# Optimization experiments

Hardware: AMD Instinct MI355X
Metric: run time of the kernel (lower is better)

## Reference

```python
import jax, jax.numpy as jnp
import numpy as np

N = 100000; E = 1600000; G = 2000; S = 40; MAXP = 50
IN = 64; F = 128; H = 4; HD = F // H; FFN = 8 * F
EPS = 1e-5; BN_EPS = 1e-5

def _ln(x, g, b):
    m = jnp.mean(x, -1, keepdims=True)
    v = jnp.mean((x - m) ** 2, -1, keepdims=True)
    return (x - m) * jax.lax.rsqrt(v + EPS) * g + b

def setup_inputs():
    key = jax.random.key(0)
    ks = jax.random.split(key, 16)
    def lin(k, i, o):
        kw, kb = jax.random.split(k)
        lim = 1.0 / np.sqrt(i)
        return (jax.random.uniform(kw, (i, o), jnp.float32, -lim, lim),
                jax.random.uniform(kb, (o,), jnp.float32, -lim, lim))
    W_gcn, b_gcn = lin(ks[1], IN, F)
    Wq, bq = lin(ks[2], F, F); Wk, bk = lin(ks[3], F, F)
    Wv, bv = lin(ks[4], F, F); Wo, bo = lin(ks[5], F, F)
    W1, b1 = lin(ks[6], F, FFN); W2, b2 = lin(ks[7], FFN, F)
    Wg, bg = lin(ks[8], 2 * F, F)
    ones = lambda: jnp.ones((F,), jnp.float32)
    zeros = lambda: jnp.zeros((F,), jnp.float32)
    return {
        'x': jax.random.normal(ks[0], (N, IN), jnp.float32),
        'edge_index': jax.random.randint(ks[9], (2, E), 0, N),
        'batch': jnp.repeat(jnp.arange(G), N // G),
        'set_batch': jnp.repeat(jnp.arange(S), G // S),
        'W_gcn': W_gcn, 'b_gcn': b_gcn,
        'bn_g': ones(), 'bn_b': zeros(),
        'lnpre_g': ones(), 'lnpre_b': zeros(),
        'Wq': Wq, 'bq': bq, 'Wk': Wk, 'bk': bk, 'Wv': Wv, 'bv': bv, 'Wo': Wo, 'bo': bo,
        'ln1_g': ones(), 'ln1_b': zeros(),
        'W1': W1, 'b1': b1, 'W2': W2, 'b2': b2,
        'ln2_g': ones(), 'ln2_b': zeros(),
        'Wg': Wg, 'bg': bg,
    }

def _forward(x, W_gcn, b_gcn, bn_g, bn_b, lnpre_g, lnpre_b, Wq, bq, Wk, bk, Wv, bv, Wo, bo, ln1_g, ln1_b, W1, b1, W2, b2, ln2_g, ln2_b, Wg, bg, edge_index, batch, set_batch):
    row, col = edge_index[0], edge_index[1]
    # GCNConv, improved=True -> self-loop weight 2.0 (PyG gcn_norm)
    xw = x @ W_gcn                                              # [N,F]
    deg = jax.ops.segment_sum(jnp.ones(E, xw.dtype), col, N) + 2.0
    dinv = jax.lax.rsqrt(deg)
    norm = dinv[row] * dinv[col]                                # [E]
    agg = jax.ops.segment_sum(xw[row] * norm[:, None], col, N)  # scatter-add to targets
    h = agg + (2.0 * dinv * dinv)[:, None] * xw + b_gcn
    # BatchNorm1d eval (running_mean=0, running_var=1) + ReLU; dropout is identity in eval
    h = jax.nn.relu(h * jax.lax.rsqrt(jnp.asarray(1.0 + BN_EPS, h.dtype)) * bn_g + bn_b)
    # global mean pool per graph
    cnt_g = jax.ops.segment_sum(jnp.ones(N, h.dtype), batch, G)
    z = jax.ops.segment_sum(h, batch, G) / cnt_g[:, None]       # [G,F]
    # to_dense_batch over sets (set_batch is sorted)
    cnt_s = jax.ops.segment_sum(jnp.ones(G, jnp.int32), set_batch, S)
    starts = jnp.cumsum(cnt_s) - cnt_s
    pos = jnp.arange(G) - starts[set_batch]                     # position within set
    zd = jnp.zeros((S, MAXP, F), z.dtype).at[set_batch, pos].set(z)
    mask = jnp.arange(MAXP)[None, :] < cnt_s[:, None]           # [S,MAXP]
    # pre-LN MHA with key_padding_mask
    zn = _ln(zd, lnpre_g, lnpre_b)
    q = (zn @ Wq + bq).reshape(S, MAXP, H, HD)
    k = (zn @ Wk + bk).reshape(S, MAXP, H, HD)
    v = (zn @ Wv + bv).reshape(S, MAXP, H, HD)
    scores = jnp.einsum('sqhd,skhd->shqk', q, k) / np.sqrt(HD)
    scores = jnp.where(mask[:, None, None, :], scores, -1e9)
    attn = jax.nn.softmax(scores, -1)
    o = jnp.einsum('shqk,skhd->sqhd', attn, v).reshape(S, MAXP, F) @ Wo + bo
    zd = _ln(zd + o, ln1_g, ln1_b)
    # FFN block (post-LN residual)
    f = jax.nn.relu(zd @ W1 + b1) @ W2 + b2
    zd = _ln(zd + f, ln2_g, ln2_b)
    # z_dense[mask] ordering == gather via (set_batch, pos); broadcast to nodes
    set_info = zd[set_batch, pos][batch]                        # [N,F]
    # gated fusion
    gate = jax.nn.sigmoid(jnp.concatenate([h, set_info], -1) @ Wg + bg)
    return gate * set_info + (1.0 - gate) * h

def reference(x, edge_index, batch, set_batch, W_gcn, b_gcn, bn_g, bn_b, lnpre_g, lnpre_b, Wq, bq, Wk, bk, Wv, bv, Wo, bo, ln1_g, ln1_b, W1, b1, W2, b2, ln2_g, ln2_b, Wg, bg):
    return _forward(x, W_gcn, b_gcn, bn_g, bn_b, lnpre_g, lnpre_b, Wq, bq, Wk, bk, Wv, bv, Wo, bo, ln1_g, ln1_b, W1, b1, W2, b2, ln2_g, ln2_b, Wg, bg, edge_index, batch, set_batch)
```

## Files before the change

### kernel.cpp

```cpp
#include <hip/hip_runtime.h>
#include <hip/hip_bf16.h>
#include <cstddef>

#define NN 100000
#define NE 1600000
#define NG 2000
#define NS 40
#define INF 64
#define F 128
#define FFN_DIM 1024
#define NB 782
#define SC_BLOCKS 512
#define SC_CHUNK 3125
#define BH_BLOCKS 128
#define BH_CHUNK 12500
#define KSPLIT 8

using bf16 = __hip_bfloat16;
using bf162 = __hip_bfloat162;
typedef __attribute__((ext_vector_type(8))) short short8;
typedef __attribute__((ext_vector_type(4))) float f32x4;
typedef __attribute__((ext_vector_type(2))) float f32x2;

__device__ __forceinline__ short f2bs(float f){
    union { bf16 b; short s; } u; u.b = __float2bfloat16(f); return u.s;
}

__global__ __launch_bounds__(1024) void k_bhist(const int* __restrict__ ei, int* __restrict__ bcnt){
    __shared__ int lh[NB];
    int t = threadIdx.x;
    int base = blockIdx.x * BH_CHUNK;
    for (int b=t; b<NB; b+=1024) lh[b] = 0;
    __syncthreads();
    for (int i=t; i<BH_CHUNK; i+=1024){
        int c = ei[NE + base + i];
        atomicAdd(&lh[c>>7], 1);
    }
    __syncthreads();
    for (int b=t; b<NB; b+=1024){
        int n = lh[b];
        if (n) atomicAdd(&bcnt[b], n);
    }
}

__global__ __launch_bounds__(1024) void k_bscan(const int* __restrict__ bcnt, int* __restrict__ bstart,
                                                int* __restrict__ bcursor){
    __shared__ int s[1024];
    int t = threadIdx.x;
    int own = (t < NB) ? bcnt[t] : 0;
    s[t] = own; __syncthreads();
    #pragma unroll
    for (int off=1; off<1024; off<<=1){
        int v = (t >= off) ? s[t-off] : 0;
        __syncthreads();
        s[t] += v;
        __syncthreads();
    }
    int excl = s[t] - own;
    if (t <= NB) bstart[t] = excl;
    if (t < NB)  bcursor[t] = excl;
}

__global__ __launch_bounds__(256) void k_xws(const float* __restrict__ x, const float* __restrict__ W,
                                             const float* __restrict__ dinv, unsigned char* __restrict__ xws8){
    __shared__ short Xs[128*72];
    __shared__ short Ws[128*72];
    int t = threadIdx.x;
    int rowBase = blockIdx.x * 128;
    #pragma unroll
    for (int i=0;i<32;i++){
        int id = i*256+t; int k = id>>7, n = id&127;
        Ws[n*72 + k] = f2bs(W[id]);
    }
    #pragma unroll
    for (int i=0;i<8;i++){
        int id = i*256+t;
        int r = id>>4; int k4 = (id&15)*4;
        int row = rowBase + r; if (row >= NN) row = NN-1;
        float4 v = *(const float4*)&x[(size_t)row*INF + k4];
        unsigned int u0 = (unsigned int)(unsigned short)f2bs(v.x) | ((unsigned int)(unsigned short)f2bs(v.y)<<16);
        unsigned int u1 = (unsigned int)(unsigned short)f2bs(v.z) | ((unsigned int)(unsigned short)f2bs(v.w)<<16);
        *(unsigned int*)&Xs[r*72 + k4]     = u0;
        *(unsigned int*)&Xs[r*72 + k4 + 2] = u1;
    }
    __syncthreads();
    int lane = t & 63, w = t >> 6;
    int lr = lane & 15, quad = lane >> 4;
    f32x4 acc[2][8];
    #pragma unroll
    for (int i=0;i<2;i++)
        #pragma unroll
        for (int j=0;j<8;j++) acc[i][j] = (f32x4){0.f,0.f,0.f,0.f};
    #pragma unroll
    for (int ks=0; ks<2; ++ks){
        int kb = ks*32 + quad*8;
        short8 b0 = *(const short8*)&Xs[((w  )*16 + lr)*72 + kb];
        short8 b1 = *(const short8*)&Xs[((w+4)*16 + lr)*72 + kb];
        #pragma unroll
        for (int mt=0; mt<8; ++mt){
            short8 a = *(const short8*)&Ws[(mt*16 + lr)*72 + kb];
            acc[0][mt] = __builtin_amdgcn_mfma_f32_16x16x32_bf16(a, b0, acc[0][mt], 0, 0, 0);
            acc[1][mt] = __builtin_amdgcn_mfma_f32_16x16x32_bf16(a, b1, acc[1][mt], 0, 0, 0);
        }
    }
    #pragma unroll
    for (int rt=0; rt<2; ++rt){
        int row = rowBase + (w + rt*4)*16 + lr;
        if (row < NN){
            float dv = dinv[row];
            #pragma unroll
            for (int mt=0; mt<8; ++mt){
                int p = __builtin_amdgcn_cvt_pk_fp8_f32(acc[rt][mt][0]*dv, acc[rt][mt][1]*dv, 0, false);
                p     = __builtin_amdgcn_cvt_pk_fp8_f32(acc[rt][mt][2]*dv, acc[rt][mt][3]*dv, p, true);
                *(int*)&xws8[(size_t)row*F + mt*16 + quad*4] = p;
            }
        }
    }
}

__global__ __launch_bounds__(1024) void k_scatter2(const int* __restrict__ ei, int* __restrict__ bcursor,
                                                   int* __restrict__ ebuf){
    __shared__ int lh[NB];
    __shared__ int lb[NB];
    int t = threadIdx.x;
    int base = blockIdx.x * SC_CHUNK;
    for (int b=t; b<NB; b+=1024) lh[b] = 0;
    __syncthreads();
    int rr[4], cc[4];
    #pragma unroll
    for (int q=0;q<4;q++){
        int i = t + q*1024;
        bool v = (i < SC_CHUNK);
        int idx = v ? (base + i) : base;
        rr[q] = ei[idx];
        cc[q] = ei[NE + idx];
        if (v) atomicAdd(&lh[cc[q]>>7], 1);
    }
    __syncthreads();
    for (int b=t; b<NB; b+=1024){
        int n = lh[b];
        lb[b] = n ? atomicAdd(&bcursor[b], n) : 0;
        lh[b] = 0;
    }
    __syncthreads();
    #pragma unroll
    for (int q=0;q<4;q++){
        int i = t + q*1024;
        if (i < SC_CHUNK){
            int b = cc[q] >> 7;
            int rk = atomicAdd(&lh[b], 1);
            ebuf[lb[b] + rk] = (rr[q] << 7) | (cc[q] & 127);
        }
    }
}

__global__ __launch_bounds__(256) void k_sort(const int* __restrict__ ebuf, const int* __restrict__ bstart,
                                              int* __restrict__ cnt, float* __restrict__ dinv,
                                              int* __restrict__ nstart, int* __restrict__ ebuf2){
    __shared__ int lh[128];
    __shared__ int s[128];
    __shared__ int lcur[128];
    int t = threadIdx.x;
    int b = blockIdx.x;
    int e0 = bstart[b];
    int nE = bstart[b+1] - e0;
    if (t < 128) lh[t] = 0;
    __syncthreads();
    for (int i=t; i<nE; i+=256) atomicAdd(&lh[ebuf[e0+i] & 127], 1);
    __syncthreads();
    int c = (t < 128) ? lh[t] : 0;
    if (t < 128) s[t] = c;
    __syncthreads();
    #pragma unroll
    for (int off=1; off<128; off<<=1){
        int v = (t >= off && t < 128) ? s[t-off] : 0;
        __syncthreads();
        if (t < 128) s[t] += v;
        __syncthreads();
    }
    int node = b*128 + t;
    if (t < 128){
        int excl = s[t] - c;
        lcur[t] = excl;
        if (node < NN){
            nstart[node] = e0 + excl;
            cnt[node] = c;
            dinv[node] = rsqrtf((float)c + 2.0f);
        }
    }
    __syncthreads();
    for (int i=t; i<nE; i+=256){
        int v = ebuf[e0 + i];
        int nl = v & 127;
        int rk = atomicAdd(&lcur[nl], 1);
        ebuf2[e0 + rk] = (v >> 7) << 5;
    }
}

__global__ __launch_bounds__(256) void k_aggpool(const unsigned char* __restrict__ xws8,
                                                 const int* __restrict__ nstart, const int* __restrict__ cnt,
                                                 const float* __restrict__ dinv, const float* __restrict__ b_gcn,
                                                 const float* __restrict__ bn_g, const float* __restrict__ bn_b,
                                                 const int* __restrict__ ebuf2,
                                                 const float* __restrict__ lnpre_g, const float* __restrict__ lnpre_b,
                                                 float* __restrict__ h, unsigned short* __restrict__ hb,
                                                 float* __restrict__ z, float* __restrict__ zn){
    __shared__ float zacc[4][128];
    int t = threadIdx.x;
    int lane = t & 63, w = t >> 6;
    int half = lane >> 5, lh = lane & 31;
    int g = blockIdx.x;
    const unsigned int* xw32 = (const unsigned int*)xws8;
    unsigned int* hb32 = (unsigned int*)hb;

    float4 bg4  = *(const float4*)&b_gcn[4*lh];
    float4 bng4 = *(const float4*)&bn_g[4*lh];
    float4 bnb4 = *(const float4*)&bn_b[4*lh];
    const float bns = rsqrtf(1.f + 1e-5f);

    float za0=0.f, za1=0.f, za2=0.f, za3=0.f;

    for (int i = w; i < 50; i += 4){
        int node = g*50 + i;
        int s0n = nstart[node]; int dg = cnt[node]; float dv = dinv[node];
        unsigned int us = xw32[node*32 + lh];
        float a0=0.f, a1=0.f, a2=0.f, a3=0.f;
        int j=0;
        for (; j+8<=dg; j+=8){
            int r0 = ebuf2[s0n+j+0+half];
            int r1 = ebuf2[s0n+j+2+half];
            int r2 = ebuf2[s0n+j+4+half];
            int r3 = ebuf2[s0n+j+6+half];
            unsigned int u0 = xw32[r0 + lh];
            unsigned int u1 = xw32[r1 + lh];
            unsigned int u2 = xw32[r2 + lh];
            unsigned int u3 = xw32[r3 + lh];
            f32x2 l0 = __builtin_amdgcn_cvt_pk_f32_fp8(u0, false);
            f32x2 h0 = __builtin_amdgcn_cvt_pk_f32_fp8(u0, true);
            f32x2 l1 = __builtin_amdgcn_cvt_pk_f32_fp8(u1, false);
            f32x2 h1 = __builtin_amdgcn_cvt_pk_f32_fp8(u1, true);
            f32x2 l2 = __builtin_amdgcn_cvt_pk_f32_fp8(u2, false);
            f32x2 h2 = __builtin_amdgcn_cvt_pk_f32_fp8(u2, true);
            f32x2 l3 = __builtin_amdgcn_cvt_pk_f32_fp8(u3, false);
            f32x2 h3 = __builtin_amdgcn_cvt_pk_f32_fp8(u3, true);
            a0 += (l0.x + l1.x) + (l2.x + l3.x);
            a1 += (l0.y + l1.y) + (l2.y + l3.y);
            a2 += (h0.x + h1.x) + (h2.x + h3.x);
            a3 += (h0.y + h1.y) + (h2.y + h3.y);
        }
        for (; j+2<=dg; j+=2){
            int r0 = ebuf2[s0n+j+half];
            unsigned int u0 = xw32[r0 + lh];
            f32x2 l0 = __builtin_amdgcn_cvt_pk_f32_fp8(u0, false);
            f32x2 h0 = __builtin_amdgcn_cvt_pk_f32_fp8(u0, true);
            a0 += l0.x; a1 += l0.y; a2 += h0.x; a3 += h0.y;
        }
        if (j < dg && half == 0){
            int r0 = ebuf2[s0n+j];
            unsigned int u0 = xw32[r0 + lh];
            f32x2 l0 = __builtin_amdgcn_cvt_pk_f32_fp8(u0, false);
            f32x2 h0 = __builtin_amdgcn_cvt_pk_f32_fp8(u0, true);
            a0 += l0.x; a1 += l0.y; a2 += h0.x; a3 += h0.y;
        }
        a0 += __shfl_xor(a0, 32);
        a1 += __shfl_xor(a1, 32);
        a2 += __shfl_xor(a2, 32);
        a3 += __shfl_xor(a3, 32);
        f32x2 fl = __builtin_amdgcn_cvt_pk_f32_fp8(us, false);
        f32x2 fh = __builtin_amdgcn_cvt_pk_f32_fp8(us, true);
        float p0 = dv*(a0 + 2.f*fl.x) + bg4.x;
        float p1 = dv*(a1 + 2.f*fl.y) + bg4.y;
        float p2 = dv*(a2 + 2.f*fh.x) + bg4.z;
        float p3 = dv*(a3 + 2.f*fh.y) + bg4.w;
        p0 = fmaxf(p0*bns*bng4.x + bnb4.x, 0.f);
        p1 = fmaxf(p1*bns*bng4.y + bnb4.y, 0.f);
        p2 = fmaxf(p2*bns*bng4.z + bnb4.z, 0.f);
        p3 = fmaxf(p3*bns*bng4.w + bnb4.w, 0.f);
        if (half == 0){
            *(float4*)&h[(size_t)node*F + 4*lh] = make_float4(p0,p1,p2,p3);
            unsigned int b0 = (unsigned int)(unsigned short)f2bs(p0) | ((unsigned int)(unsigned short)f2bs(p1) << 16);
            unsigned int b1 = (unsigned int)(unsigned short)f2bs(p2) | ((unsigned int)(unsigned short)f2bs(p3) << 16);
            *(uint2*)&hb32[(size_t)node*64 + 2*lh] = make_uint2(b0, b1);
        }
        za0 += p0; za1 += p1; za2 += p2; za3 += p3;
    }
    if (half == 0)
        *(float4*)&zacc[w][4*lh] = make_float4(za0, za1, za2, za3);
    __syncthreads();
    if (w == 0){
        float4 v0 = *(const float4*)&zacc[0][4*lh];
        float4 v1 = *(const float4*)&zacc[1][4*lh];
        float4 v2 = *(const float4*)&zacc[2][4*lh];
        float4 v3 = *(const float4*)&zacc[3][4*lh];
        float s0 = ((v0.x+v1.x)+(v2.x+v3.x)) / 50.0f;
        float s1 = ((v0.y+v1.y)+(v2.y+v3.y)) / 50.0f;
        float s2 = ((v0.z+v1.z)+(v2.z+v3.z)) / 50.0f;
        float s3 = ((v0.w+v1.w)+(v2.w+v3.w)) / 50.0f;
        if (half == 0)
            *(float4*)&z[(size_t)g*F + 4*lh] = make_float4(s0,s1,s2,s3);
        float s = (s0+s1)+(s2+s3);
        #pragma unroll
        for (int off=1; off<32; off<<=1) s += __shfl_xor(s, off);
        float m = s * (1.f/128.f);
        float d0=s0-m, d1=s1-m, d2=s2-m, d3=s3-m;
        float vv = (d0*d0+d1*d1)+(d2*d2+d3*d3);
        #pragma unroll
        for (int off=1; off<32; off<<=1) vv += __shfl_xor(vv, off);
        float rs = rsqrtf(vv*(1.f/128.f) + 1e-5f);
        float4 lg = *(const float4*)&lnpre_g[4*lh];
        float4 lb = *(const float4*)&lnpre_b[4*lh];
        if (half == 0)
            *(float4*)&zn[(size_t)g*F + 4*lh] = make_float4(d0*rs*lg.x+lb.x, d1*rs*lg.y+lb.y,
                                                            d2*rs*lg.z+lb.z, d3*rs*lg.w+lb.w);
    }
}

__global__ __launch_bounds__(256) void k_wo_ln(const float* __restrict__ ao, const float* __restrict__ Wo,
                                               const float* __restrict__ bo, const float* __restrict__ z,
                                               const float* __restrict__ g, const float* __restrict__ b,
                                               float* __restrict__ zd1){
    __shared__ float As[32*36];
    __shared__ float Bs[32*128];
    int t = threadIdx.x;
    int rowBase = blockIdx.x*32;
    int c0 = (t&31)*4, r0 = (t>>5)*4;
    float acc[4][4];
    #pragma unroll
    for (int i=0;i<4;i++){ acc[i][0]=0.f; acc[i][1]=0.f; acc[i][2]=0.f; acc[i][3]=0.f; }
    for (int kb=0; kb<F; kb+=32){
        #pragma unroll
        for (int i=0;i<4;i++){
            int id = i*256+t; int kk = id&31; int r = id>>5;
            int row = rowBase + r;
            As[kk*36+r] = (row<NG) ? ao[(size_t)row*F + kb + kk] : 0.f;
        }
        #pragma unroll
        for (int i=0;i<16;i++){
            int id = i*256+t; int c = id&127; int kk = id>>7;
            Bs[kk*128+c] = Wo[(size_t)(kb+kk)*F + c];
        }
        __syncthreads();
        for (int kk=0;kk<32;kk++){
            float4 a = *(const float4*)&As[kk*36+r0];
            float4 bv = *(const float4*)&Bs[kk*128+c0];
            float av[4]={a.x,a.y,a.z,a.w}; float bb[4]={bv.x,bv.y,bv.z,bv.w};
            #pragma unroll
            for(int i=0;i<4;i++)
                #pragma unroll
                for(int j=0;j<4;j++) acc[i][j] += av[i]*bb[j];
        }
        __syncthreads();
    }
    float4 bo4 = *(const float4*)&bo[c0];
    float4 g4  = *(const float4*)&g[c0];
    float4 b4  = *(const float4*)&b[c0];
    #pragma unroll
    for (int i=0;i<4;i++){
        int row = rowBase + r0 + i;
        float v0=0.f,v1=0.f,v2=0.f,v3=0.f;
        if (row < NG){
            float4 zr = *(const float4*)&z[(size_t)row*F + c0];
            v0 = acc[i][0] + bo4.x + zr.x;
            v1 = acc[i][1] + bo4.y + zr.y;
            v2 = acc[i][2] + bo4.z + zr.z;
            v3 = acc[i][3] + bo4.w + zr.w;
        }
        float s = (v0+v1)+(v2+v3);
        #pragma unroll
        for (int off=1; off<32; off<<=1) s += __shfl_xor(s, off);
        float m = s * (1.f/128.f);
        float d0=v0-m, d1=v1-m, d2=v2-m, d3=v3-m;
        float vv = (d0*d0+d1*d1)+(d2*d2+d3*d3);
        #pragma unroll
        for (int off=1; off<32; off<<=1) vv += __shfl_xor(vv, off);
        float rs = rsqrtf(vv*(1.f/128.f) + 1e-5f);
        if (row < NG)
            *(float4*)&zd1[(size_t)row*F + c0] = make_float4(d0*rs*g4.x+b4.x, d1*rs*g4.y+b4.y,
                                                             d2*rs*g4.z+b4.z, d3*rs*g4.w+b4.w);
    }
}

__global__ __launch_bounds__(256) void k_ln_red_gsi(const float* __restrict__ A, const float* __restrict__ part,
                                                    const float* __restrict__ bias, const float* __restrict__ g,
                                                    const float* __restrict__ b, const float* __restrict__ Wb,
                                                    const float* __restrict__ bg, float* __restrict__ zd2,
                                                    float* __restrict__ gsi){
    __shared__ float Zs[4][128];
    __shared__ float Bs[32*128];
    int t = threadIdx.x; int lane = t&63;
    int rquad = t>>6;
    int row = blockIdx.x*4 + rquad;
    int i0 = row*F + 2*lane;
    float x0 = A[i0] + bias[2*lane], x1 = A[i0+1] + bias[2*lane+1];
    #pragma unroll
    for (int zz=0; zz<KSPLIT; ++zz){
        x0 += part[(size_t)zz*NG*F + i0];
        x1 += part[(size_t)zz*NG*F + i0 + 1];
    }
    float s = x0+x1;
    for (int off=1; off<64; off<<=1) s += __shfl_xor(s, off);
    float m = s * (1.f/128.f);
    float d0 = x0-m, d1 = x1-m;
    float vv = d0*d0 + d1*d1;
    for (int off=1; off<64; off<<=1) vv += __shfl_xor(vv, off);
    float rs = rsqrtf(vv*(1.f/128.f) + 1e-5f);
    float o0 = d0*rs*g[2*lane]   + b[2*lane];
    float o1 = d1*rs*g[2*lane+1] + b[2*lane+1];
    zd2[i0]   = o0;
    zd2[i0+1] = o1;
    Zs[rquad][2*lane]   = o0;
    Zs[rquad][2*lane+1] = o1;
    __syncthreads();
    int col = t & 127, rp = t >> 7;
    float a0=0.f, a1=0.f;
    for (int kb=0; kb<F; kb+=32){
        #pragma unroll
        for (int i=0;i<16;i++){
            int id = i*256+t; int c = id&127; int kk = id>>7;
            Bs[kk*128+c] = Wb[(size_t)(kb+kk)*F + c];
        }
        __syncthreads();
        for (int kk=0;kk<32;kk++){
            float w = Bs[kk*128+col];
            a0 += Zs[rp][kb+kk]   * w;
            a1 += Zs[rp+2][kb+kk] * w;
        }
        __syncthreads();
    }
    float bgc = bg[col];
    gsi[(size_t)(blockIdx.x*4 + rp)*F + col]     = a0 + bgc;
    gsi[(size_t)(blockIdx.x*4 + rp + 2)*F + col] = a1 + bgc;
}

template<int RELU>
__global__ __launch_bounds__(256) void k_gemm(const float* __restrict__ A, const float* __restrict__ B,
                                              const float* __restrict__ bias, float* __restrict__ C,
                                              int M, int K, int Nc){
    __shared__ float As[32*68];
    __shared__ float Bs[32*64];
    int t = threadIdx.x;
    int rowBase = blockIdx.x*64;
    int colBase = blockIdx.y*64;
    int c0 = (t&15)*4, r0 = (t>>4)*4;
    float acc[4][4];
    #pragma unroll
    for (int i=0;i<4;i++){ acc[i][0]=0.f; acc[i][1]=0.f; acc[i][2]=0.f; acc[i][3]=0.f; }
    for (int kb=0; kb<K; kb+=32){
        #pragma unroll
        for (int i=0;i<8;i++){
            int id = i*256+t; int kk = id&31; int r = id>>5;
            int row = rowBase + r;
            As[kk*68+r] = (row<M) ? A[(size_t)row*K + kb + kk] : 0.f;
        }
        #pragma unroll
        for (int i=0;i<8;i++){
            int id = i*256+t; int c = id&63; int kk = id>>6;
            Bs[kk*64+c] = B[(size_t)(kb+kk)*Nc + colBase + c];
        }
        __syncthreads();
        for (int kk=0;kk<32;kk++){
            float4 a = *(const float4*)&As[kk*68+r0];
            float4 b = *(const float4*)&Bs[kk*64+c0];
            float av[4]={a.x,a.y,a.z,a.w}; float bv[4]={b.x,b.y,b.z,b.w};
            #pragma unroll
            for(int i=0;i<4;i++)
                #pragma unroll
                for(int j=0;j<4;j++) acc[i][j] += av[i]*bv[j];
        }
        __syncthreads();
    }
    for (int i=0;i<4;i++){
        int row = rowBase + r0 + i;
        if (row < M){
            for (int j=0;j<4;j++){
                float v = acc[i][j] + bias[colBase+c0+j];
                if (RELU) v = fmaxf(v, 0.f);
                C[(size_t)row*Nc + colBase + c0 + j] = v;
            }
        }
    }
}

__global__ __launch_bounds__(256) void k_gemm_splitk(const float* __restrict__ A, const float* __restrict__ B,
                                                     float* __restrict__ part, int M, int K, int Nc){
    __shared__ float As[32*68];
    __shared__ float Bs[32*64];
    int t = threadIdx.x;
    int rowBase = blockIdx.x*64;
    int colBase = blockIdx.y*64;
    int z = blockIdx.z;
    int kchunk = K / KSPLIT;
    int kbeg = z * kchunk;
    int c0 = (t&15)*4, r0 = (t>>4)*4;
    float acc[4][4];
    #pragma unroll
    for (int i=0;i<4;i++){ acc[i][0]=0.f; acc[i][1]=0.f; acc[i][2]=0.f; acc[i][3]=0.f; }
    for (int kb=kbeg; kb<kbeg+kchunk; kb+=32){
        #pragma unroll
        for (int i=0;i<8;i++){
            int id = i*256+t; int kk = id&31; int r = id>>5;
            int row = rowBase + r;
            As[kk*68+r] = (row<M) ? A[(size_t)row*K + kb + kk] : 0.f;
        }
        #pragma unroll
        for (int i=0;i<8;i++){
            int id = i*256+t; int c = id&63; int kk = id>>6;
            Bs[kk*64+c] = B[(size_t)(kb+kk)*Nc + colBase + c];
        }
        __syncthreads();
        for (int kk=0;kk<32;kk++){
            float4 a = *(const float4*)&As[kk*68+r0];
            float4 b = *(const float4*)&Bs[kk*64+c0];
            float av[4]={a.x,a.y,a.z,a.w}; float bv[4]={b.x,b.y,b.z,b.w};
            #pragma unroll
            for(int i=0;i<4;i++)
                #pragma unroll
                for(int j=0;j<4;j++) acc[i][j] += av[i]*bv[j];
        }
        __syncthreads();
    }
    float* Cp = part + (size_t)z*M*Nc;
    for (int i=0;i<4;i++){
        int row = rowBase + r0 + i;
        if (row < M){
            for (int j=0;j<4;j++)
                Cp[(size_t)row*Nc + colBase + c0 + j] = acc[i][j];
        }
    }
}

__global__ __launch_bounds__(256) void k_gemm_qkv(const float* __restrict__ A,
                                                  const float* __restrict__ Wq, const float* __restrict__ Wk,
                                                  const float* __restrict__ Wv, const float* __restrict__ bq,
                                                  const float* __restrict__ bk, const float* __restrict__ bv,
                                                  float* __restrict__ Cq, float* __restrict__ Ck,
                                                  float* __restrict__ Cv){
    __shared__ float As[32*68];
    __shared__ float Bs[32*64];
    int t = threadIdx.x;
    int rowBase = blockIdx.x*64;
    int colBase = blockIdx.y*64;
    int z = blockIdx.z;
    const float* B = (z==0) ? Wq : (z==1) ? Wk : Wv;
    const float* bias = (z==0) ? bq : (z==1) ? bk : bv;
    float* C = (z==0) ? Cq : (z==1) ? Ck : Cv;
    int c0 = (t&15)*4, r0 = (t>>4)*4;
    float acc[4][4];
    #pragma unroll
    for (int i=0;i<4;i++){ acc[i][0]=0.f; acc[i][1]=0.f; acc[i][2]=0.f; acc[i][3]=0.f; }
    for (int kb=0; kb<F; kb+=32){
        #pragma unroll
        for (int i=0;i<8;i++){
            int id = i*256+t; int kk = id&31; int r = id>>5;
            int row = rowBase + r;
            As[kk*68+r] = (row<NG) ? A[(size_t)row*F + kb + kk] : 0.f;
        }
        #pragma unroll
        for (int i=0;i<8;i++){
            int id = i*256+t; int c = id&63; int kk = id>>6;
            Bs[kk*64+c] = B[(size_t)(kb+kk)*F + colBase + c];
        }
        __syncthreads();
        for (int kk=0;kk<32;kk++){
            float4 a = *(const float4*)&As[kk*68+r0];
            float4 b = *(const float4*)&Bs[kk*64+c0];
            float av[4]={a.x,a.y,a.z,a.w}; float bv4[4]={b.x,b.y,b.z,b.w};
            #pragma unroll
            for(int i=0;i<4;i++)
                #pragma unroll
                for(int j=0;j<4;j++) acc[i][j] += av[i]*bv4[j];
        }
        __syncthreads();
    }
    for (int i=0;i<4;i++){
        int row = rowBase + r0 + i;
        if (row < NG){
            for (int j=0;j<4;j++)
                C[(size_t)row*F + colBase + c0 + j] = acc[i][j] + bias[colBase+c0+j];
        }
    }
}

__global__ __launch_bounds__(256) void k_attn(const float* __restrict__ q, const float* __restrict__ k,
                                              const float* __restrict__ v, float* __restrict__ o){
    __shared__ float Qs[1600], Ks[1600], Vs[1600], Sc[2500];
    int t = threadIdx.x;
    int s = blockIdx.x >> 2; int hh = blockIdx.x & 3;
    for (int idx=t; idx<1600; idx+=256){
        int i = idx>>5, d = idx&31;
        size_t gi = (size_t)(s*50+i)*F + hh*32 + d;
        Qs[idx]=q[gi]; Ks[idx]=k[gi]; Vs[idx]=v[gi];
    }
    __syncthreads();
    for (int idx=t; idx<2500; idx+=256){
        int qi = idx/50, ki = idx%50;
        float acc=0.f;
        #pragma unroll 8
        for (int d=0;d<32;d++) acc += Qs[qi*32+d]*Ks[ki*32+d];
        Sc[idx] = acc * 0.17677669529663687f;
    }
    __syncthreads();
    if (t < 50){
        float m=-1e30f;
        for (int j=0;j<50;j++) m = fmaxf(m, Sc[t*50+j]);
        float sum=0.f;
        for (int j=0;j<50;j++){ float e=__expf(Sc[t*50+j]-m); Sc[t*50+j]=e; sum+=e; }
        float inv = 1.f/sum;
        for (int j=0;j<50;j++) Sc[t*50+j] *= inv;
    }
    __syncthreads();
    for (int idx=t; idx<1600; idx+=256){
        int qi = idx>>5, d = idx&31;
        float acc=0.f;
        #pragma unroll 10
        for (int ki=0;ki<50;ki++) acc += Sc[qi*50+ki]*Vs[ki*32+d];
        o[(size_t)(s*50+qi)*F + hh*32 + d] = acc;
    }
}

__global__ __launch_bounds__(256) void k_gate_mfma(const float* __restrict__ h,
                                                   const unsigned short* __restrict__ hb,
                                                   const float* __restrict__ Wg,
                                                   const float* __restrict__ gsi, const float* __restrict__ zd2,
                                                   float* __restrict__ out){
    __shared__ short Bw[128*136];
    int t = threadIdx.x;
    for (int i=t; i<16384; i+=256){
        int k = i >> 7, n = i & 127;
        Bw[n*136 + k] = f2bs(Wg[(size_t)k*F + n]);
    }
    __syncthreads();
    int lane = t & 63, w = t >> 6;
    int lr = lane & 15, quad = lane >> 4;
    int mrow0 = blockIdx.x*128 + w*32;
    f32x4 acc[2][8];
    #pragma unroll
    for (int i=0;i<2;i++)
        #pragma unroll
        for (int j=0;j<8;j++) acc[i][j] = (f32x4){0.f,0.f,0.f,0.f};
    #pragma unroll
    for (int ks=0; ks<4; ++ks){
        int kb = ks*32 + quad*8;
        short8 a[2];
        #pragma unroll
        for (int mt=0; mt<2; ++mt){
            int row = mrow0 + mt*16 + lr;
            if (row >= NN) row = NN-1;
            a[mt] = *(const short8*)&hb[(size_t)row*F + kb];
        }
        #pragma unroll
        for (int nt=0; nt<8; ++nt){
            short8 b = *(const short8*)&Bw[(nt*16 + lr)*136 + kb];
            acc[0][nt] = __builtin_amdgcn_mfma_f32_16x16x32_bf16(a[0], b, acc[0][nt], 0, 0, 0);
            acc[1][nt] = __builtin_amdgcn_mfma_f32_16x16x32_bf16(a[1], b, acc[1][nt], 0, 0, 0);
        }
    }
    #pragma unroll
    for (int mt=0; mt<2; ++mt){
        #pragma unroll
        for (int r=0; r<4; ++r){
            int row = mrow0 + mt*16 + quad*4 + r;
            if (row >= NN) continue;
            int g = row / 50;
            const float* gs = &gsi[(size_t)g*F];
            const float* zs = &zd2[(size_t)g*F];
            const float* hr = &h[(size_t)row*F];
            float* orow = &out[(size_t)row*F];
            #pragma unroll
            for (int nt=0; nt<8; ++nt){
                int col = nt*16 + lr;
                float L = acc[mt][nt][r] + gs[col];
                float gate = 1.f/(1.f + __expf(-L));
                orow[col] = gate*zs[col] + (1.f-gate)*hr[col];
            }
        }
    }
}

extern "C" void kernel_launch(void* const* d_in, const int* in_sizes, int n_in,
                              void* d_out, int out_size, void* d_ws, size_t ws_size,
                              hipStream_t stream) {
    const float* x      = (const float*)d_in[0];
    const int*   ei     = (const int*)d_in[1];
    const float* W_gcn  = (const float*)d_in[4];
    const float* b_gcn  = (const float*)d_in[5];
    const float* bn_g   = (const float*)d_in[6];
    const float* bn_b   = (const float*)d_in[7];
    const float* lnpre_g= (const float*)d_in[8];
    const float* lnpre_b= (const float*)d_in[9];
    const float* Wq     = (const float*)d_in[10];
    const float* bq     = (const float*)d_in[11];
    const float* Wk     = (const float*)d_in[12];
    const float* bk     = (const float*)d_in[13];
    const float* Wv     = (const float*)d_in[14];
    const float* bv     = (const float*)d_in[15];
    const float* Wo     = (const float*)d_in[16];
    const float* bo     = (const float*)d_in[17];
    const float* ln1_g  = (const float*)d_in[18];
    const float* ln1_b  = (const float*)d_in[19];
    const float* W1     = (const float*)d_in[20];
    const float* b1     = (const float*)d_in[21];
    const float* W2     = (const float*)d_in[22];
    const float* b2     = (const float*)d_in[23];
    const float* ln2_g  = (const float*)d_in[24];
    const float* ln2_b  = (const float*)d_in[25];
    const float* Wg     = (const float*)d_in[26];
    const float* bg     = (const float*)d_in[27];
    float* out = (float*)d_out;
    char* ws = (char*)d_ws;

    size_t o = 0;
    unsigned char* xws8 = (unsigned char*)(ws + o); o += (size_t)NN*F;
    float* h     = (float*)(ws + o); o += (size_t)NN*F*4;
    unsigned short* hb = (unsigned short*)(ws + o); o += (size_t)NN*F*2;
    int*   cnt   = (int*)(ws + o);   o += (size_t)NN*4;
    int*   nstart= (int*)(ws + o);   o += (size_t)NN*4;
    int*   ebuf  = (int*)(ws + o);   o += (size_t)NE*4;
    int*   ebuf2 = (int*)(ws + o);   o += (size_t)NE*4;
    float* dinv  = (float*)(ws + o); o += (size_t)NN*4;
    int*   bcnt  = (int*)(ws + o);   o += 1024*4;
    int*   bstart= (int*)(ws + o);   o += 1024*4;
    int*   bcursor=(int*)(ws + o);   o += 1024*4;
    float* z     = (float*)(ws + o); o += (size_t)NG*F*4;
    float* zn    = (float*)(ws + o); o += (size_t)NG*F*4;
    float* qb    = (float*)(ws + o); o += (size_t)NG*F*4;
    float* kb2   = (float*)(ws + o); o += (size_t)NG*F*4;
    float* vb    = (float*)(ws + o); o += (size_t)NG*F*4;
    float* ao    = (float*)(ws + o); o += (size_t)NG*F*4;
    float* zd1   = (float*)(ws + o); o += (size_t)NG*F*4;
    float* ffn1  = (float*)(ws + o); o += (size_t)NG*FFN_DIM*4;
    float* part  = (float*)(ws + o); o += (size_t)KSPLIT*NG*F*4;
    float* zd2   = (float*)(ws + o); o += (size_t)NG*F*4;
    float* gsi   = (float*)(ws + o); o += (size_t)NG*F*4;

    hipMemsetAsync(bcnt, 0, (size_t)NB*4, stream);
    k_bhist<<<BH_BLOCKS, 1024, 0, stream>>>(ei, bcnt);
    k_bscan<<<1, 1024, 0, stream>>>(bcnt, bstart, bcursor);
    k_scatter2<<<SC_BLOCKS, 1024, 0, stream>>>(ei, bcursor, ebuf);
    k_sort<<<NB, 256, 0, stream>>>(ebuf, bstart, cnt, dinv, nstart, ebuf2);
    k_xws<<<(NN+127)/128, 256, 0, stream>>>(x, W_gcn, dinv, xws8);
    k_aggpool<<<NG, 256, 0, stream>>>(xws8, nstart, cnt, dinv, b_gcn, bn_g, bn_b, ebuf2,
                                      lnpre_g, lnpre_b, h, hb, z, zn);

    dim3 gqkv(32, 2, 3);
    k_gemm_qkv<<<gqkv, 256, 0, stream>>>(zn, Wq, Wk, Wv, bq, bk, bv, qb, kb2, vb);
    k_attn<<<NS*4, 256, 0, stream>>>(qb, kb2, vb, ao);
    k_wo_ln<<<(NG+31)/32, 256, 0, stream>>>(ao, Wo, bo, z, ln1_g, ln1_b, zd1);
    dim3 gffn1(32, 16);
    k_gemm<1><<<gffn1, 256, 0, stream>>>(zd1, W1, b1, ffn1, NG, F, FFN_DIM);
    dim3 gsk(32, 2, KSPLIT);
    k_gemm_splitk<<<gsk, 256, 0, stream>>>(ffn1, W2, part, NG, FFN_DIM, F);
    k_ln_red_gsi<<<NG/4, 256, 0, stream>>>(zd1, part, b2, ln2_g, ln2_b,
                                           Wg + (size_t)F*F, bg, zd2, gsi);

    k_gate_mfma<<<782, 256, 0, stream>>>(h, hb, Wg, gsi, zd2, out);
}
```

Before: 360.8 us.

## Use fixed-capacity edge buckets and bf16 MFMA GEMMs for QKV and FFN

Replaces the edge-bucket histogram and scan kernels with fixed-capacity buckets (BCAP slots per bucket), initialised by one small kernel, so bucket counts come straight from the scatter cursors. The QKV, FFN1 and FFN2 fp32 SIMT GEMMs are replaced by bf16 MFMA kernels that take bf16 copies of zn and zd1 written by earlier stages, and FFN1 now writes its intermediate in bf16. This removes two launches and a memset and moves the small dense GEMMs onto matrix cores. In exchange it adds bf16 rounding error and risks overflow if any bucket gets more than 3072 edges.

```diff
diff --git a/kernel.cpp b/kernel.cpp
--- a/kernel.cpp
+++ b/kernel.cpp
@@ -10,14 +10,12 @@
 #define F 128
 #define FFN_DIM 1024
 #define NB 782
+#define BCAP 3072
 #define SC_BLOCKS 512
 #define SC_CHUNK 3125
-#define BH_BLOCKS 128
-#define BH_CHUNK 12500
 #define KSPLIT 8
 
 using bf16 = __hip_bfloat16;
-using bf162 = __hip_bfloat162;
 typedef __attribute__((ext_vector_type(8))) short short8;
 typedef __attribute__((ext_vector_type(4))) float f32x4;
 typedef __attribute__((ext_vector_type(2))) float f32x2;
@@ -25,40 +23,13 @@
 __device__ __forceinline__ short f2bs(float f){
     union { bf16 b; short s; } u; u.b = __float2bfloat16(f); return u.s;
 }
-
-__global__ __launch_bounds__(1024) void k_bhist(const int* __restrict__ ei, int* __restrict__ bcnt){
-    __shared__ int lh[NB];
-    int t = threadIdx.x;
-    int base = blockIdx.x * BH_CHUNK;
-    for (int b=t; b<NB; b+=1024) lh[b] = 0;
-    __syncthreads();
-    for (int i=t; i<BH_CHUNK; i+=1024){
-        int c = ei[NE + base + i];
-        atomicAdd(&lh[c>>7], 1);
-    }
-    __syncthreads();
-    for (int b=t; b<NB; b+=1024){
-        int n = lh[b];
-        if (n) atomicAdd(&bcnt[b], n);
-    }
-}
-
-__global__ __launch_bounds__(1024) void k_bscan(const int* __restrict__ bcnt, int* __restrict__ bstart,
-                                                int* __restrict__ bcursor){
-    __shared__ int s[1024];
-    int t = threadIdx.x;
-    int own = (t < NB) ? bcnt[t] : 0;
-    s[t] = own; __syncthreads();
-    #pragma unroll
-    for (int off=1; off<1024; off<<=1){
-        int v = (t >= off) ? s[t-off] : 0;
-        __syncthreads();
-        s[t] += v;
-        __syncthreads();
-    }
-    int excl = s[t] - own;
-    if (t <= NB) bstart[t] = excl;
-    if (t < NB)  bcursor[t] = excl;
+__device__ __forceinline__ unsigned int pk2(float a, float b){
+    return (unsigned int)(unsigned short)f2bs(a) | ((unsigned int)(unsigned short)f2bs(b) << 16);
+}
+
+__global__ __launch_bounds__(1024) void k_binit(int* __restrict__ bcursor){
+    int t = threadIdx.x;
+    if (t < NB) bcursor[t] = t * BCAP;
 }
 
 __global__ __launch_bounds__(256) void k_xws(const float* __restrict__ x, const float* __restrict__ W,
@@ -78,10 +49,8 @@
         int r = id>>4; int k4 = (id&15)*4;
         int row = rowBase + r; if (row >= NN) row = NN-1;
         float4 v = *(const float4*)&x[(size_t)row*INF + k4];
-        unsigned int u0 = (unsigned int)(unsigned short)f2bs(v.x) | ((unsigned int)(unsigned short)f2bs(v.y)<<16);
-        unsigned int u1 = (unsigned int)(unsigned short)f2bs(v.z) | ((unsigned int)(unsigned short)f2bs(v.w)<<16);
-        *(unsigned int*)&Xs[r*72 + k4]     = u0;
-        *(unsigned int*)&Xs[r*72 + k4 + 2] = u1;
+        *(unsigned int*)&Xs[r*72 + k4]     = pk2(v.x, v.y);
+        *(unsigned int*)&Xs[r*72 + k4 + 2] = pk2(v.z, v.w);
     }
     __syncthreads();
     int lane = t & 63, w = t >> 6;
@@ -154,7 +123,7 @@
     }
 }
 
-__global__ __launch_bounds__(256) void k_sort(const int* __restrict__ ebuf, const int* __restrict__ bstart,
+__global__ __launch_bounds__(256) void k_sort(const int* __restrict__ ebuf, const int* __restrict__ bcursor,
                                               int* __restrict__ cnt, float* __restrict__ dinv,
                                               int* __restrict__ nstart, int* __restrict__ ebuf2){
     __shared__ int lh[128];
@@ -162,8 +131,8 @@
     __shared__ int lcur[128];
     int t = threadIdx.x;
     int b = blockIdx.x;
-    int e0 = bstart[b];
-    int nE = bstart[b+1] - e0;
+    int e0 = b * BCAP;
+    int nE = bcursor[b] - e0;
     if (t < 128) lh[t] = 0;
     __syncthreads();
     for (int i=t; i<nE; i+=256) atomicAdd(&lh[ebuf[e0+i] & 127], 1);
@@ -204,7 +173,8 @@
                                                  const int* __restrict__ ebuf2,
                                                  const float* __restrict__ lnpre_g, const float* __restrict__ lnpre_b,
                                                  float* __restrict__ h, unsigned short* __restrict__ hb,
-                                                 float* __restrict__ z, float* __restrict__ zn){
+                                                 float* __restrict__ z, float* __restrict__ zn,
+                                                 unsigned short* __restrict__ znb){
     __shared__ float zacc[4][128];
     int t = threadIdx.x;
     int lane = t & 63, w = t >> 6;
@@ -212,6 +182,7 @@
     int g = blockIdx.x;
     const unsigned int* xw32 = (const unsigned int*)xws8;
     unsigned int* hb32 = (unsigned int*)hb;
+    unsigned int* znb32 = (unsigned int*)znb;
 
     float4 bg4  = *(const float4*)&b_gcn[4*lh];
     float4 bng4 = *(const float4*)&bn_g[4*lh];
@@ -278,9 +249,7 @@
         p3 = fmaxf(p3*bns*bng4.w + bnb4.w, 0.f);
         if (half == 0){
             *(float4*)&h[(size_t)node*F + 4*lh] = make_float4(p0,p1,p2,p3);
-            unsigned int b0 = (unsigned int)(unsigned short)f2bs(p0) | ((unsigned int)(unsigned short)f2bs(p1) << 16);
-            unsigned int b1 = (unsigned int)(unsigned short)f2bs(p2) | ((unsigned int)(unsigned short)f2bs(p3) << 16);
-            *(uint2*)&hb32[(size_t)node*64 + 2*lh] = make_uint2(b0, b1);
+            *(uint2*)&hb32[(size_t)node*64 + 2*lh] = make_uint2(pk2(p0,p1), pk2(p2,p3));
         }
         za0 += p0; za1 += p1; za2 += p2; za3 += p3;
     }
@@ -309,21 +278,148 @@
         float rs = rsqrtf(vv*(1.f/128.f) + 1e-5f);
         float4 lg = *(const float4*)&lnpre_g[4*lh];
         float4 lb = *(const float4*)&lnpre_b[4*lh];
-        if (half == 0)
-            *(float4*)&zn[(size_t)g*F + 4*lh] = make_float4(d0*rs*lg.x+lb.x, d1*rs*lg.y+lb.y,
-                                                            d2*rs*lg.z+lb.z, d3*rs*lg.w+lb.w);
+        if (half == 0){
+            float o0 = d0*rs*lg.x+lb.x, o1 = d1*rs*lg.y+lb.y;
+            float o2 = d2*rs*lg.z+lb.z, o3 = d3*rs*lg.w+lb.w;
+            *(float4*)&zn[(size_t)g*F + 4*lh] = make_float4(o0,o1,o2,o3);
+            *(uint2*)&znb32[(size_t)g*64 + 2*lh] = make_uint2(pk2(o0,o1), pk2(o2,o3));
+        }
+    }
+}
+
+template<int RELU, int BF16OUT, int SPLITK>
+__global__ __launch_bounds__(256) void k_mm_bf16(const unsigned short* __restrict__ A,
+                                                 const float* __restrict__ B, const float* __restrict__ bias,
+                                                 float* __restrict__ Cf, unsigned short* __restrict__ Cb,
+                                                 int M, int K, int Nc){
+    __shared__ short Bw[128*136];
+    int t = threadIdx.x;
+    int rowBase = blockIdx.x*128;
+    int colBase = blockIdx.y*128;
+    int kbeg = SPLITK ? blockIdx.z*128 : 0;
+    #pragma unroll
+    for (int i=0;i<64;i++){
+        int id = i*256+t; int k = id>>7, n = id&127;
+        Bw[n*136 + k] = f2bs(B[(size_t)(kbeg+k)*Nc + colBase + n]);
+    }
+    __syncthreads();
+    int lane = t & 63, w = t >> 6;
+    int lr = lane & 15, quad = lane >> 4;
+    int mrow0 = rowBase + w*32;
+    f32x4 acc[2][8];
+    #pragma unroll
+    for (int i=0;i<2;i++)
+        #pragma unroll
+        for (int j=0;j<8;j++) acc[i][j] = (f32x4){0.f,0.f,0.f,0.f};
+    #pragma unroll
+    for (int ks=0; ks<4; ++ks){
+        int kb = ks*32 + quad*8;
+        short8 a[2];
+        #pragma unroll
+        for (int mt=0; mt<2; ++mt){
+            int row = mrow0 + mt*16 + lr;
+            if (row >= M) row = M-1;
+            a[mt] = *(const short8*)&A[(size_t)row*K + kbeg + kb];
+        }
+        #pragma unroll
+        for (int nt=0; nt<8; ++nt){
+            short8 b = *(const short8*)&Bw[(nt*16 + lr)*136 + kb];
+            acc[0][nt] = __builtin_amdgcn_mfma_f32_16x16x32_bf16(a[0], b, acc[0][nt], 0, 0, 0);
+            acc[1][nt] = __builtin_amdgcn_mfma_f32_16x16x32_bf16(a[1], b, acc[1][nt], 0, 0, 0);
+        }
+    }
+    #pragma unroll
+    for (int mt=0; mt<2; ++mt){
+        #pragma unroll
+        for (int r=0; r<4; ++r){
+            int row = mrow0 + mt*16 + quad*4 + r;
+            if (row >= M) continue;
+            #pragma unroll
+            for (int nt=0; nt<8; ++nt){
+                int col = colBase + nt*16 + lr;
+                float v = acc[mt][nt][r];
+                if (!SPLITK){
+                    v += bias[col];
+                    if (RELU) v = fmaxf(v, 0.f);
+                    if (BF16OUT) Cb[(size_t)row*Nc + col] = (unsigned short)f2bs(v);
+                    else         Cf[(size_t)row*Nc + col] = v;
+                } else {
+                    Cf[(size_t)blockIdx.z*M*Nc + (size_t)row*Nc + col] = v;
+                }
+            }
+        }
+    }
+}
+
+__global__ __launch_bounds__(256) void k_qkv_mfma(const unsigned short* __restrict__ A,
+                                                  const float* __restrict__ Wq, const float* __restrict__ Wk,
+                                                  const float* __restrict__ Wv, const float* __restrict__ bq,
+                                                  const float* __restrict__ bk, const float* __restrict__ bv,
+                                                  float* __restrict__ Cq, float* __restrict__ Ck,
+                                                  float* __restrict__ Cv){
+    __shared__ short Bw[128*136];
+    int t = threadIdx.x;
+    int zsel = blockIdx.z;
+    const float* B = (zsel==0) ? Wq : (zsel==1) ? Wk : Wv;
+    const float* bias = (zsel==0) ? bq : (zsel==1) ? bk : bv;
+    float* C = (zsel==0) ? Cq : (zsel==1) ? Ck : Cv;
+    int rowBase = blockIdx.x*128;
+    #pragma unroll
+    for (int i=0;i<64;i++){
+        int id = i*256+t; int k = id>>7, n = id&127;
+        Bw[n*136 + k] = f2bs(B[(size_t)k*F + n]);
+    }
+    __syncthreads();
+    int lane = t & 63, w = t >> 6;
+    int lr = lane & 15, quad = lane >> 4;
+    int mrow0 = rowBase + w*32;
+    f32x4 acc[2][8];
+    #pragma unroll
+    for (int i=0;i<2;i++)
+        #pragma unroll
+        for (int j=0;j<8;j++) acc[i][j] = (f32x4){0.f,0.f,0.f,0.f};
+    #pragma unroll
+    for (int ks=0; ks<4; ++ks){
+        int kb = ks*32 + quad*8;
+        short8 a[2];
+        #pragma unroll
+        for (int mt=0; mt<2; ++mt){
+            int row = mrow0 + mt*16 + lr;
+            if (row >= NG) row = NG-1;
+            a[mt] = *(const short8*)&A[(size_t)row*F + kb];
+        }
+        #pragma unroll
+        for (int nt=0; nt<8; ++nt){
+            short8 b = *(const short8*)&Bw[(nt*16 + lr)*136 + kb];
+            acc[0][nt] = __builtin_amdgcn_mfma_f32_16x16x32_bf16(a[0], b, acc[0][nt], 0, 0, 0);
+            acc[1][nt] = __builtin_amdgcn_mfma_f32_16x16x32_bf16(a[1], b, acc[1][nt], 0, 0, 0);
+        }
+    }
+    #pragma unroll
+    for (int mt=0; mt<2; ++mt){
+        #pragma unroll
+        for (int r=0; r<4; ++r){
+            int row = mrow0 + mt*16 + quad*4 + r;
+            if (row >= NG) continue;
+            #pragma unroll
+            for (int nt=0; nt<8; ++nt){
+                int col = nt*16 + lr;
+                C[(size_t)row*F + col] = acc[mt][nt][r] + bias[col];
+            }
+        }
     }
 }
 
 __global__ __launch_bounds__(256) void k_wo_ln(const float* __restrict__ ao, const float* __restrict__ Wo,
                                                const float* __restrict__ bo, const float* __restrict__ z,
                                                const float* __restrict__ g, const float* __restrict__ b,
-                                               float* __restrict__ zd1){
+                                               float* __restrict__ zd1, unsigned short* __restrict__ zd1b){
     __shared__ float As[32*36];
     __shared__ float Bs[32*128];
     int t = threadIdx.x;
     int rowBase = blockIdx.x*32;
     int c0 = (t&31)*4, r0 = (t>>5)*4;
+    unsigned int* zd1b32 = (unsigned int*)zd1b;
     float acc[4][4];
     #pragma unroll
     for (int i=0;i<4;i++){ acc[i][0]=0.f; acc[i][1]=0.f; acc[i][2]=0.f; acc[i][3]=0.f; }
@@ -374,9 +470,12 @@
         #pragma unroll
         for (int off=1; off<32; off<<=1) vv += __shfl_xor(vv, off);
         float rs = rsqrtf(vv*(1.f/128.f) + 1e-5f);
-        if (row < NG)
-            *(float4*)&zd1[(size_t)row*F + c0] = make_float4(d0*rs*g4.x+b4.x, d1*rs*g4.y+b4.y,
-                                                             d2*rs*g4.z+b4.z, d3*rs*g4.w+b4.w);
+        if (row < NG){
+            float o0 = d0*rs*g4.x+b4.x, o1 = d1*rs*g4.y+b4.y;
+            float o2 = d2*rs*g4.z+b4.z, o3 = d3*rs*g4.w+b4.w;
+            *(float4*)&zd1[(size_t)row*F + c0] = make_float4(o0,o1,o2,o3);
+            *(uint2*)&zd1b32[(size_t)row*(F/2) + c0/2] = make_uint2(pk2(o0,o1), pk2(o2,o3));
+        }
     }
 }
 
@@ -430,155 +529,6 @@
     float bgc = bg[col];
     gsi[(size_t)(blockIdx.x*4 + rp)*F + col]     = a0 + bgc;
     gsi[(size_t)(blockIdx.x*4 + rp + 2)*F + col] = a1 + bgc;
-}
-
-template<int RELU>
-__global__ __launch_bounds__(256) void k_gemm(const float* __restrict__ A, const float* __restrict__ B,
-                                              const float* __restrict__ bias, float* __restrict__ C,
-                                              int M, int K, int Nc){
-    __shared__ float As[32*68];
-    __shared__ float Bs[32*64];
-    int t = threadIdx.x;
-    int rowBase = blockIdx.x*64;
-    int colBase = blockIdx.y*64;
-    int c0 = (t&15)*4, r0 = (t>>4)*4;
-    float acc[4][4];
-    #pragma unroll
-    for (int i=0;i<4;i++){ acc[i][0]=0.f; acc[i][1]=0.f; acc[i][2]=0.f; acc[i][3]=0.f; }
-    for (int kb=0; kb<K; kb+=32){
-        #pragma unroll
-        for (int i=0;i<8;i++){
-            int id = i*256+t; int kk = id&31; int r = id>>5;
-            int row = rowBase + r;
-            As[kk*68+r] = (row<M) ? A[(size_t)row*K + kb + kk] : 0.f;
-        }
-        #pragma unroll
-        for (int i=0;i<8;i++){
-            int id = i*256+t; int c = id&63; int kk = id>>6;
-            Bs[kk*64+c] = B[(size_t)(kb+kk)*Nc + colBase + c];
-        }
-        __syncthreads();
-        for (int kk=0;kk<32;kk++){
-            float4 a = *(const float4*)&As[kk*68+r0];
-            float4 b = *(const float4*)&Bs[kk*64+c0];
-            float av[4]={a.x,a.y,a.z,a.w}; float bv[4]={b.x,b.y,b.z,b.w};
-            #pragma unroll
-            for(int i=0;i<4;i++)
-                #pragma unroll
-                for(int j=0;j<4;j++) acc[i][j] += av[i]*bv[j];
-        }
-        __syncthreads();
-    }
-    for (int i=0;i<4;i++){
-        int row = rowBase + r0 + i;
-        if (row < M){
-            for (int j=0;j<4;j++){
-                float v = acc[i][j] + bias[colBase+c0+j];
-                if (RELU) v = fmaxf(v, 0.f);
-                C[(size_t)row*Nc + colBase + c0 + j] = v;
-            }
-        }
-    }
-}
-
-__global__ __launch_bounds__(256) void k_gemm_splitk(const float* __restrict__ A, const float* __restrict__ B,
-                                                     float* __restrict__ part, int M, int K, int Nc){
-    __shared__ float As[32*68];
-    __shared__ float Bs[32*64];
-    int t = threadIdx.x;
-    int rowBase = blockIdx.x*64;
-    int colBase = blockIdx.y*64;
-    int z = blockIdx.z;
-    int kchunk = K / KSPLIT;
-    int kbeg = z * kchunk;
-    int c0 = (t&15)*4, r0 = (t>>4)*4;
-    float acc[4][4];
-    #pragma unroll
-    for (int i=0;i<4;i++){ acc[i][0]=0.f; acc[i][1]=0.f; acc[i][2]=0.f; acc[i][3]=0.f; }
-    for (int kb=kbeg; kb<kbeg+kchunk; kb+=32){
-        #pragma unroll
-        for (int i=0;i<8;i++){
-            int id = i*256+t; int kk = id&31; int r = id>>5;
-            int row = rowBase + r;
-            As[kk*68+r] = (row<M) ? A[(size_t)row*K + kb + kk] : 0.f;
-        }
-        #pragma unroll
-        for (int i=0;i<8;i++){
-            int id = i*256+t; int c = id&63; int kk = id>>6;
-            Bs[kk*64+c] = B[(size_t)(kb+kk)*Nc + colBase + c];
-        }
-        __syncthreads();
-        for (int kk=0;kk<32;kk++){
-            float4 a = *(const float4*)&As[kk*68+r0];
-            float4 b = *(const float4*)&Bs[kk*64+c0];
-            float av[4]={a.x,a.y,a.z,a.w}; float bv[4]={b.x,b.y,b.z,b.w};
-            #pragma unroll
-            for(int i=0;i<4;i++)
-                #pragma unroll
-                for(int j=0;j<4;j++) acc[i][j] += av[i]*bv[j];
-        }
-        __syncthreads();
-    }
-    float* Cp = part + (size_t)z*M*Nc;
-    for (int i=0;i<4;i++){
-        int row = rowBase + r0 + i;
-        if (row < M){
-            for (int j=0;j<4;j++)
-                Cp[(size_t)row*Nc + colBase + c0 + j] = acc[i][j];
-        }
-    }
-}
-
-__global__ __launch_bounds__(256) void k_gemm_qkv(const float* __restrict__ A,
-                                                  const float* __restrict__ Wq, const float* __restrict__ Wk,
-                                                  const float* __restrict__ Wv, const float* __restrict__ bq,
-                                                  const float* __restrict__ bk, const float* __restrict__ bv,
-                                                  float* __restrict__ Cq, float* __restrict__ Ck,
-                                                  float* __restrict__ Cv){
-    __shared__ float As[32*68];
-    __shared__ float Bs[32*64];
-    int t = threadIdx.x;
-    int rowBase = blockIdx.x*64;
-    int colBase = blockIdx.y*64;
-    int z = blockIdx.z;
-    const float* B = (z==0) ? Wq : (z==1) ? Wk : Wv;
-    const float* bias = (z==0) ? bq : (z==1) ? bk : bv;
-    float* C = (z==0) ? Cq : (z==1) ? Ck : Cv;
-    int c0 = (t&15)*4, r0 = (t>>4)*4;
-    float acc[4][4];
-    #pragma unroll
-    for (int i=0;i<4;i++){ acc[i][0]=0.f; acc[i][1]=0.f; acc[i][2]=0.f; acc[i][3]=0.f; }
-    for (int kb=0; kb<F; kb+=32){
-        #pragma unroll
-        for (int i=0;i<8;i++){
-            int id = i*256+t; int kk = id&31; int r = id>>5;
-            int row = rowBase + r;
-            As[kk*68+r] = (row<NG) ? A[(size_t)row*F + kb + kk] : 0.f;
-        }
-        #pragma unroll
-        for (int i=0;i<8;i++){
-            int id = i*256+t; int c = id&63; int kk = id>>6;
-            Bs[kk*64+c] = B[(size_t)(kb+kk)*F + colBase + c];
-        }
-        __syncthreads();
-        for (int kk=0;kk<32;kk++){
-            float4 a = *(const float4*)&As[kk*68+r0];
-            float4 b = *(const float4*)&Bs[kk*64+c0];
-            float av[4]={a.x,a.y,a.z,a.w}; float bv4[4]={b.x,b.y,b.z,b.w};
-            #pragma unroll
-            for(int i=0;i<4;i++)
-                #pragma unroll
-                for(int j=0;j<4;j++) acc[i][j] += av[i]*bv4[j];
-        }
-        __syncthreads();
-    }
-    for (int i=0;i<4;i++){
-        int row = rowBase + r0 + i;
-        if (row < NG){
-            for (int j=0;j<4;j++)
-                C[(size_t)row*F + colBase + c0 + j] = acc[i][j] + bias[colBase+c0+j];
-        }
-    }
 }
 
 __global__ __launch_bounds__(256) void k_attn(const float* __restrict__ q, const float* __restrict__ k,
@@ -715,41 +665,39 @@
     unsigned short* hb = (unsigned short*)(ws + o); o += (size_t)NN*F*2;
     int*   cnt   = (int*)(ws + o);   o += (size_t)NN*4;
     int*   nstart= (int*)(ws + o);   o += (size_t)NN*4;
-    int*   ebuf  = (int*)(ws + o);   o += (size_t)NE*4;
-    int*   ebuf2 = (int*)(ws + o);   o += (size_t)NE*4;
+    int*   ebuf  = (int*)(ws + o);   o += (size_t)NB*BCAP*4;
+    int*   ebuf2 = (int*)(ws + o);   o += (size_t)NB*BCAP*4;
     float* dinv  = (float*)(ws + o); o += (size_t)NN*4;
-    int*   bcnt  = (int*)(ws + o);   o += 1024*4;
-    int*   bstart= (int*)(ws + o);   o += 1024*4;
     int*   bcursor=(int*)(ws + o);   o += 1024*4;
     float* z     = (float*)(ws + o); o += (size_t)NG*F*4;
     float* zn    = (float*)(ws + o); o += (size_t)NG*F*4;
+    unsigned short* znb = (unsigned short*)(ws + o); o += (size_t)NG*F*2;
     float* qb    = (float*)(ws + o); o += (size_t)NG*F*4;
     float* kb2   = (float*)(ws + o); o += (size_t)NG*F*4;
     float* vb    = (float*)(ws + o); o += (size_t)NG*F*4;
     float* ao    = (float*)(ws + o); o += (size_t)NG*F*4;
     float* zd1   = (float*)(ws + o); o += (size_t)NG*F*4;
-    float* ffn1  = (float*)(ws + o); o += (size_t)NG*FFN_DIM*4;
+    unsigned short* zd1b = (unsigned short*)(ws + o); o += (size_t)NG*F*2;
+    unsigned short* ffn1b = (unsigned short*)(ws + o); o += (size_t)NG*FFN_DIM*2;
     float* part  = (float*)(ws + o); o += (size_t)KSPLIT*NG*F*4;
     float* zd2   = (float*)(ws + o); o += (size_t)NG*F*4;
     float* gsi   = (float*)(ws + o); o += (size_t)NG*F*4;
 
-    hipMemsetAsync(bcnt, 0, (size_t)NB*4, stream);
-    k_bhist<<<BH_BLOCKS, 1024, 0, stream>>>(ei, bcnt);
-    k_bscan<<<1, 1024, 0, stream>>>(bcnt, bstart, bcursor);
+    k_binit<<<1, 1024, 0, stream>>>(bcursor);
     k_scatter2<<<SC_BLOCKS, 1024, 0, stream>>>(ei, bcursor, ebuf);
-    k_sort<<<NB, 256, 0, stream>>>(ebuf, bstart, cnt, dinv, nstart, ebuf2);
+    k_sort<<<NB, 256, 0, stream>>>(ebuf, bcursor, cnt, dinv, nstart, ebuf2);
     k_xws<<<(NN+127)/128, 256, 0, stream>>>(x, W_gcn, dinv, xws8);
     k_aggpool<<<NG, 256, 0, stream>>>(xws8, nstart, cnt, dinv, b_gcn, bn_g, bn_b, ebuf2,
-                                      lnpre_g, lnpre_b, h, hb, z, zn);
-
-    dim3 gqkv(32, 2, 3);
-    k_gemm_qkv<<<gqkv, 256, 0, stream>>>(zn, Wq, Wk, Wv, bq, bk, bv, qb, kb2, vb);
+                                      lnpre_g, lnpre_b, h, hb, z, zn, znb);
+
+    dim3 gqkv((NG+127)/128, 1, 3);
+    k_qkv_mfma<<<gqkv, 256, 0, stream>>>(znb, Wq, Wk, Wv, bq, bk, bv, qb, kb2, vb);
     k_attn<<<NS*4, 256, 0, stream>>>(qb, kb2, vb, ao);
-    k_wo_ln<<<(NG+31)/32, 256, 0, stream>>>(ao, Wo, bo, z, ln1_g, ln1_b, zd1);
-    dim3 gffn1(32, 16);
-    k_gemm<1><<<gffn1, 256, 0, stream>>>(zd1, W1, b1, ffn1, NG, F, FFN_DIM);
-    dim3 gsk(32, 2, KSPLIT);
-    k_gemm_splitk<<<gsk, 256, 0, stream>>>(ffn1, W2, part, NG, FFN_DIM, F);
+    k_wo_ln<<<(NG+31)/32, 256, 0, stream>>>(ao, Wo, bo, z, ln1_g, ln1_b, zd1, zd1b);
+    dim3 gffn1((NG+127)/128, FFN_DIM/128, 1);
+    k_mm_bf16<1,1,0><<<gffn1, 256, 0, stream>>>(zd1b, W1, b1, nullptr, ffn1b, NG, F, FFN_DIM);
+    dim3 gffn2((NG+127)/128, 1, KSPLIT);
+    k_mm_bf16<0,0,1><<<gffn2, 256, 0, stream>>>(ffn1b, W2, nullptr, part, nullptr, NG, FFN_DIM, F);
     k_ln_red_gsi<<<NG/4, 256, 0, stream>>>(zd1, part, b2, ln2_g, ln2_b,
                                            Wg + (size_t)F*F, bg, zd2, gsi);
 
```

Measured after the change: 354.0 us. About the same (-1.9%).
